# Optimization experiments

Hardware: AMD Instinct MI355X
Metric: run time of the kernel (lower is better)

## Reference

```python
import jax, jax.numpy as jnp
import numpy as np

D_MODEL = 768
D_FF = 3072
N_BEHAVIORS = 4
EPS = 1e-12


def layer_norm(x, g, b):
    m = jnp.mean(x, axis=-1, keepdims=True)
    v = jnp.mean(jnp.square(x - m), axis=-1, keepdims=True)
    return (x - m) * jax.lax.rsqrt(v + EPS) * g + b


def setup_inputs() -> dict:
    key = jax.random.key(0)
    ks = jax.random.split(key, 8)
    B, L = 8, 2048
    s1 = 1.0 / np.sqrt(D_MODEL)
    s2 = 1.0 / np.sqrt(D_FF)
    return {
        "input_tensor": jax.random.normal(ks[0], (B, L, D_MODEL), dtype=jnp.float32),
        "type_seq": jax.random.randint(ks[1], (B, L), 0, N_BEHAVIORS + 1),
        # per-behavior FeedForward params, stacked on leading n dim
        "W1": jax.random.normal(ks[2], (N_BEHAVIORS, D_MODEL, D_FF), dtype=jnp.float32) * s1,
        "b1": jnp.zeros((N_BEHAVIORS, D_FF), dtype=jnp.float32),
        "W2": jax.random.normal(ks[3], (N_BEHAVIORS, D_FF, D_MODEL), dtype=jnp.float32) * s2,
        "b2": jnp.zeros((N_BEHAVIORS, D_MODEL), dtype=jnp.float32),
        "ln_g": jnp.ones((N_BEHAVIORS, D_MODEL), dtype=jnp.float32),
        "ln_b": jnp.zeros((N_BEHAVIORS, D_MODEL), dtype=jnp.float32),
        # outer LayerNorm params
        "out_g": jnp.ones((D_MODEL,), dtype=jnp.float32),
        "out_b": jnp.zeros((D_MODEL,), dtype=jnp.float32),
    }


def reference(input_tensor, type_seq, W1, b1, W2, b2, ln_g, ln_b, out_g, out_b):
    n = W1.shape[0]
    # run every behavior's FeedForward over the full sequence (dense over-compute)
    h = jnp.einsum('BLH,nHF->nBLF', input_tensor, W1) + b1[:, None, None, :]
    h = jax.nn.gelu(h, approximate=False)  # torch 'gelu' = exact erf form
    h = jnp.einsum('nBLF,nFH->nBLH', h, W2) + b2[:, None, None, :]
    # per-expert residual LayerNorm (FeedForward with residual=True)
    h = layer_norm(h + input_tensor[None], ln_g[:, None, None, :], ln_b[:, None, None, :])
    # prepend zeros branch (class 0 = padding) then one-hot select per token
    stacked = jnp.concatenate([jnp.zeros_like(input_tensor)[None], h], axis=0)  # [n+1,B,L,H]
    onehot = jax.nn.one_hot(type_seq, n + 1, dtype=input_tensor.dtype)  # [B,L,n+1]
    sel = jnp.einsum('nBLH,BLn->BLH', stacked, onehot)
    # dropout is identity in eval; fused residual + LayerNorm
    return layer_norm(sel + input_tensor, out_g, out_b)
```

## Files before the change

kernel.cpp:

```cpp
#include <hip/hip_runtime.h>
#include <hip/hip_bf16.h>
#include <math.h>

#define NTOK   16384
#define DM     768
#define DF     3072
#define NEXP   4

#define RBLKS  64
#define XBLKS  768
#define WBLKS  288
#define PREP_BLKS (RBLKS + XBLKS + 2 * WBLKS)

typedef short bf16x8 __attribute__((ext_vector_type(8)));
typedef float f32x4  __attribute__((ext_vector_type(4)));

#define WS_CNT    0u
#define WS_BASES  256u
#define WS_POS    512u
#define WS_LIST   (512u + 65536u)
#define WS_XB     (WS_LIST + 262144u)
#define WS_W1T    (WS_XB + 25165824u)
#define WS_W2T    (WS_W1T + 18874368u)
#define WS_H1     (WS_W2T + 18874368u)
#define WS_H2     (WS_H1 + 100663296u)
#define WS_END    (WS_H2 + 25165824u)

__device__ __forceinline__ ushort f2bf(float f) {
    unsigned int v; __builtin_memcpy(&v, &f, 4);
    v = v + 0x7fffu + ((v >> 16) & 1u);
    return (ushort)(v >> 16);
}
__device__ __forceinline__ float bf2f(ushort u) {
    unsigned int v = ((unsigned int)u) << 16;
    float f; __builtin_memcpy(&f, &v, 4); return f;
}

__device__ __forceinline__ float fast_gelu(float v) {
    float y = v + 0.044715f * v * v * v;
    float e = __builtin_amdgcn_exp2f(-2.3022082f * y);
    return v * __builtin_amdgcn_rcpf(1.0f + e);
}

typedef __attribute__((address_space(1))) const void gvoid_t;
typedef __attribute__((address_space(3))) void lvoid_t;
__device__ __forceinline__ void cp16(const void* g, void* l) {
    __builtin_amdgcn_global_load_lds((gvoid_t*)g, (lvoid_t*)l, 16, 0, 0);
}

__device__ __forceinline__ int xcd_remap(int id, int T) {
    const int q = T >> 3, r = T & 7;
    const int x = id & 7, j = id >> 3;
    return (x < r ? x * (q + 1) : r * (q + 1) + (x - r) * q) + j;
}

__device__ __forceinline__ void transpose_tile(
    const float* __restrict__ src, ushort* __restrict__ dst, int R, int C,
    int bx, int by, int tid, ushort* tile ) {
    const int r0 = by * 64, c0 = bx * 64;
#pragma unroll
    for (int q = 0; q < 2; ++q) {
        int li = q * 256 + tid;
        int r = li >> 3, c = (li & 7) * 8;
        const float* s = src + (size_t)(r0 + r) * C + (c0 + c);
        float4 v0 = *(const float4*)s;
        float4 v1 = *(const float4*)(s + 4);
        ushort tmp[8];
        tmp[0] = f2bf(v0.x); tmp[1] = f2bf(v0.y); tmp[2] = f2bf(v0.z); tmp[3] = f2bf(v0.w);
        tmp[4] = f2bf(v1.x); tmp[5] = f2bf(v1.y); tmp[6] = f2bf(v1.z); tmp[7] = f2bf(v1.w);
        int sw = (((c >> 3) ^ ((r >> 3) & 7)) << 3);
        *(uint4*)&tile[r * 72 + sw] = *(uint4*)tmp;
    }
    __syncthreads();
#pragma unroll
    for (int q = 0; q < 2; ++q) {
        int li = q * 256 + tid;
        int r = li >> 3, c = (li & 7) * 8;
        ushort tmp[8];
#pragma unroll
        for (int j = 0; j < 8; ++j)
            tmp[j] = tile[(c + j) * 72 +
                          ((((r >> 3) & 7) ^ (((c + j) >> 3) & 7)) << 3) + (r & 7)];
        *(uint4*)(dst + (size_t)(c0 + r) * R + (r0 + c)) = *(uint4*)tmp;
    }
}

__global__ __launch_bounds__(256) void prep_kernel(
    const int* __restrict__ type_seq, const float* __restrict__ X,
    const float* __restrict__ W1, const float* __restrict__ W2,
    int* __restrict__ cnt,
    int* __restrict__ pos_of, int* __restrict__ list,
    ushort* __restrict__ Xb, ushort* __restrict__ W1t, ushort* __restrict__ W2t) {
    __shared__ ushort tile[64 * 72];
    __shared__ int lcnt[NEXP];
    __shared__ int lbase[NEXP];
    const int tid = threadIdx.x;
    const int bid = blockIdx.x;

    if (bid < RBLKS) {
        if (tid < NEXP) lcnt[tid] = 0;
        __syncthreads();
        const int lane = tid & 63;
        const int t = bid * 256 + tid;
        const int k = type_seq[t];
        int my_e = -1, my_p = 0;
#pragma unroll
        for (int e = 0; e < NEXP; ++e) {
            unsigned long long m = __ballot(k == e + 1);
            int total = __popcll(m);
            int b = 0;
            if (lane == 0 && total) b = atomicAdd(&lcnt[e], total);
            b = __shfl(b, 0, 64);
            if (k == e + 1) {
                my_e = e;
                my_p = b + __popcll(m & ((1ull << lane) - 1ull));
            }
        }
        __syncthreads();
        if (tid < NEXP && lcnt[tid] > 0)
            lbase[tid] = atomicAdd(&cnt[tid], lcnt[tid]);
        __syncthreads();
        if (my_e >= 0) {
            int gp = lbase[my_e] + my_p;
            list[my_e * NTOK + gp] = t;
            pos_of[t] = gp;
        }
        return;
    }

    int id = bid - RBLKS;
    if (id < XBLKS) {
        size_t ibase = ((size_t)id * 8 * 256 + tid) * 8;
        float4 va[8], vb[8];
#pragma unroll
        for (int k = 0; k < 8; ++k) {
            va[k] = *(const float4*)(X + ibase + (size_t)k * 2048);
            vb[k] = *(const float4*)(X + ibase + (size_t)k * 2048 + 4);
        }
#pragma unroll
        for (int k = 0; k < 8; ++k) {
            ushort tmp[8];
            tmp[0] = f2bf(va[k].x); tmp[1] = f2bf(va[k].y);
            tmp[2] = f2bf(va[k].z); tmp[3] = f2bf(va[k].w);
            tmp[4] = f2bf(vb[k].x); tmp[5] = f2bf(vb[k].y);
            tmp[6] = f2bf(vb[k].z); tmp[7] = f2bf(vb[k].w);
            *(uint4*)(Xb + ibase + (size_t)k * 2048) = *(uint4*)tmp;
        }
        return;
    }
    id -= XBLKS;
    if (id < WBLKS) {
#pragma unroll 1
        for (int k = 0; k < 8; ++k) {
            int tt = id * 8 + k;
            int z = tt / 576, rr = tt % 576;
            size_t mb = (size_t)z * DM * DF;
            transpose_tile(W1 + mb, W1t + mb, DM, DF, rr % 48, rr / 48, tid, tile);
            __syncthreads();
        }
        return;
    }
    id -= WBLKS;
    {
#pragma unroll 1
        for (int k = 0; k < 8; ++k) {
            int tt = id * 8 + k;
            int z = tt / 576, rr = tt % 576;
            size_t mb = (size_t)z * DF * DM;
            transpose_tile(W2 + mb, W2t + mb, DF, DM, rr % 12, rr / 12, tid, tile);
            __syncthreads();
        }
    }
}

__global__ __launch_bounds__(64) void scan_kernel(
    const int* __restrict__ cnt, int* __restrict__ bases) {
    if (threadIdx.x == 0) {
        int s = 0, mb = 0;
        for (int e = 0; e < NEXP; ++e) {
            bases[e] = s;
            bases[8 + e] = mb;
            s += cnt[e];
            mb += (cnt[e] + 127) >> 7;
        }
        bases[12] = mb;
    }
}


__global__ __launch_bounds__(512, 4) void gemm1_kernel(
    const ushort* __restrict__ Xb, const ushort* __restrict__ W1t,
    const float* __restrict__ b1, const int* __restrict__ cnt,
    const int* __restrict__ bases, const int* __restrict__ list,
    ushort* __restrict__ h1) {
    const int mb = bases[12];
    const int T = mb * 24;
    int id = blockIdx.y * 24 + blockIdx.x;
    if (id >= T) return;
    id = xcd_remap(id, T);
    const int y = id / 24;
    const int n0 = (id % 24) * 128;
    const int* mboff = bases + 8;
    const int e = (y >= mboff[1]) + (y >= mboff[2]) + (y >= mboff[3]);
    const int m0 = (y - mboff[e]) << 7;
    const int count = cnt[e];
    const int NK = DM / 32;

    __shared__ __align__(16) short As[3][4096];
    __shared__ __align__(16) short Bs[3][4096];

    const int tid = threadIdx.x;
    const int wave = tid >> 6, lane = tid & 63;
    const int wm = (wave & 1) * 64, wn = (wave >> 1) * 32;
    const int lrow = lane & 15;
    const int qg = lane >> 4;

    int r0 = min(m0 + (tid >> 2), count - 1);
    int t0 = list[e * NTOK + r0];
    const int qsrc = ((tid & 3) ^ ((tid >> 3) & 3)) * 8;
    const ushort* a0 = Xb + (size_t)t0 * DM + qsrc;
    const ushort* Wb = W1t + (size_t)e * DF * DM;
    const ushort* bp0 = Wb + (size_t)(n0 + (tid >> 2)) * DM + qsrc;

    int aOff[4], bOff[2];
#pragma unroll
    for (int i = 0; i < 4; ++i) {
        int ra = wm + i * 16 + lrow;
        aOff[i] = ra * 32 + (qg ^ ((ra >> 1) & 3)) * 8;
    }
#pragma unroll
    for (int j = 0; j < 2; ++j) {
        int rb = wn + j * 16 + lrow;
        bOff[j] = rb * 32 + (qg ^ ((rb >> 1) & 3)) * 8;
    }

    f32x4 z = {0.f, 0.f, 0.f, 0.f};
    f32x4 acc[4][2];
#pragma unroll
    for (int i = 0; i < 4; ++i)
#pragma unroll
        for (int j = 0; j < 2; ++j) acc[i][j] = z;

    auto STAGE = [&](int wb) {
        cp16(a0, &As[0][0] + wb * 4096 + tid * 8);
        cp16(bp0, &Bs[0][0] + wb * 4096 + tid * 8);
        a0 += 32; bp0 += 32;
    };

    STAGE(0); STAGE(1);
    int rb = 0;
    for (int ks = 0; ks < NK; ++ks) {
        __builtin_amdgcn_sched_barrier(0);
        if (ks + 1 < NK) { asm volatile("s_waitcnt vmcnt(2)" ::: "memory"); }
        else             { asm volatile("s_waitcnt vmcnt(0)" ::: "memory"); }
        __builtin_amdgcn_s_barrier();
        __builtin_amdgcn_sched_barrier(0);
        if (ks + 2 < NK) {
            int wb = rb - 1; if (wb < 0) wb += 3;
            STAGE(wb);
        }
        const short* Ab = &As[0][0] + rb * 4096;
        const short* Bb = &Bs[0][0] + rb * 4096;
        bf16x8 av[4], bv[2];
#pragma unroll
        for (int i = 0; i < 4; ++i) av[i] = *(const bf16x8*)(Ab + aOff[i]);
#pragma unroll
        for (int j = 0; j < 2; ++j) bv[j] = *(const bf16x8*)(Bb + bOff[j]);
#pragma unroll
        for (int i = 0; i < 4; ++i)
#pragma unroll
            for (int j = 0; j < 2; ++j)
                acc[i][j] = __builtin_amdgcn_mfma_f32_16x16x32_bf16(av[i], bv[j], acc[i][j], 0, 0, 0);
        rb = (rb + 1 == 3) ? 0 : rb + 1;
    }

    const int base = bases[e];
    float bias[2];
#pragma unroll
    for (int nt = 0; nt < 2; ++nt)
        bias[nt] = b1[e * DF + n0 + wn + nt * 16 + lrow];
#pragma unroll
    for (int mt = 0; mt < 4; ++mt) {
        int gm = m0 + wm + mt * 16 + (lane >> 4) * 4;
#pragma unroll
        for (int nt = 0; nt < 2; ++nt) {
            int gn = n0 + wn + nt * 16 + lrow;
#pragma unroll
            for (int r = 0; r < 4; ++r) {
                int i = gm + r;
                if (i < count) {
                    float v = acc[mt][nt][r] + bias[nt];
                    h1[(size_t)(base + i) * DF + gn] = f2bf(fast_gelu(v));
                }
            }
        }
    }
}

__global__ __launch_bounds__(512, 4) void gemm2_kernel(
    const ushort* __restrict__ h1, const ushort* __restrict__ W2t,
    const float* __restrict__ b2, const int* __restrict__ cnt,
    const int* __restrict__ bases, ushort* __restrict__ h2) {
    const int mb = bases[12];
    const int T = mb * 6;
    int id = blockIdx.y * 6 + blockIdx.x;
    if (id >= T) return;
    id = xcd_remap(id, T);
    const int y = id / 6;
    const int n0 = (id % 6) * 128;
    const int* mboff = bases + 8;
    const int e = (y >= mboff[1]) + (y >= mboff[2]) + (y >= mboff[3]);
    const int m0 = (y - mboff[e]) << 7;
    const int count = cnt[e];
    const int base = bases[e];
    const int NK = DF / 32;

    __shared__ __align__(16) short As[3][4096];
    __shared__ __align__(16) short Bs[3][4096];

    const int tid = threadIdx.x;
    const int wave = tid >> 6, lane = tid & 63;
    const int wm = (wave & 1) * 64, wn = (wave >> 1) * 32;
    const int lrow = lane & 15;
    const int qg = lane >> 4;

    int r0 = min(m0 + (tid >> 2), count - 1);
    const int qsrc = ((tid & 3) ^ ((tid >> 3) & 3)) * 8;
    const ushort* a0 = h1 + (size_t)(base + r0) * DF + qsrc;
    const ushort* Wb = W2t + (size_t)e * DM * DF;
    const ushort* bp0 = Wb + (size_t)(n0 + (tid >> 2)) * DF + qsrc;

    int aOff[4], bOff[2];
#pragma unroll
    for (int i = 0; i < 4; ++i) {
        int ra = wm + i * 16 + lrow;
        aOff[i] = ra * 32 + (qg ^ ((ra >> 1) & 3)) * 8;
    }
#pragma unroll
    for (int j = 0; j < 2; ++j) {
        int rb = wn + j * 16 + lrow;
        bOff[j] = rb * 32 + (qg ^ ((rb >> 1) & 3)) * 8;
    }

    f32x4 z = {0.f, 0.f, 0.f, 0.f};
    f32x4 acc[4][2];
#pragma unroll
    for (int i = 0; i < 4; ++i)
#pragma unroll
        for (int j = 0; j < 2; ++j) acc[i][j] = z;

    auto STAGE = [&](int wb) {
        cp16(a0, &As[0][0] + wb * 4096 + tid * 8);
        cp16(bp0, &Bs[0][0] + wb * 4096 + tid * 8);
        a0 += 32; bp0 += 32;
    };

    STAGE(0); STAGE(1);
    int rb = 0;
    for (int ks = 0; ks < NK; ++ks) {
        __builtin_amdgcn_sched_barrier(0);
        if (ks + 1 < NK) { asm volatile("s_waitcnt vmcnt(2)" ::: "memory"); }
        else             { asm volatile("s_waitcnt vmcnt(0)" ::: "memory"); }
        __builtin_amdgcn_s_barrier();
        __builtin_amdgcn_sched_barrier(0);
        if (ks + 2 < NK) {
            int wb = rb - 1; if (wb < 0) wb += 3;
            STAGE(wb);
        }
        const short* Ab = &As[0][0] + rb * 4096;
        const short* Bb = &Bs[0][0] + rb * 4096;
        bf16x8 av[4], bv[2];
#pragma unroll
        for (int i = 0; i < 4; ++i) av[i] = *(const bf16x8*)(Ab + aOff[i]);
#pragma unroll
        for (int j = 0; j < 2; ++j) bv[j] = *(const bf16x8*)(Bb + bOff[j]);
#pragma unroll
        for (int i = 0; i < 4; ++i)
#pragma unroll
            for (int j = 0; j < 2; ++j)
                acc[i][j] = __builtin_amdgcn_mfma_f32_16x16x32_bf16(av[i], bv[j], acc[i][j], 0, 0, 0);
        rb = (rb + 1 == 3) ? 0 : rb + 1;
    }

    float bias[2];
#pragma unroll
    for (int nt = 0; nt < 2; ++nt)
        bias[nt] = b2[e * DM + n0 + wn + nt * 16 + lrow];
#pragma unroll
    for (int mt = 0; mt < 4; ++mt) {
        int gm = m0 + wm + mt * 16 + (lane >> 4) * 4;
#pragma unroll
        for (int nt = 0; nt < 2; ++nt) {
            int gn = n0 + wn + nt * 16 + lrow;
#pragma unroll
            for (int r = 0; r < 4; ++r) {
                int i = gm + r;
                if (i < count)
                    h2[(size_t)(base + i) * DM + gn] = f2bf(acc[mt][nt][r] + bias[nt]);
            }
        }
    }
}

__global__ __launch_bounds__(256) void finalize_kernel(
    const float* __restrict__ X, const int* __restrict__ type_seq,
    const int* __restrict__ pos_of, const int* __restrict__ bases,
    const ushort* __restrict__ h2,
    const float* __restrict__ ln_g, const float* __restrict__ ln_b,
    const float* __restrict__ out_g, const float* __restrict__ out_b,
    float* __restrict__ out) {
    const int tid = threadIdx.x;
    const int wave = tid >> 6, lane = tid & 63;
    const int col0 = lane * 4;

#pragma unroll 1
    for (int ti = 0; ti < 2; ++ti) {
        const int t = blockIdx.x * 8 + wave * 2 + ti;
        const int k = type_seq[t];

        const float* Xr = X + (size_t)t * DM;
        float4 xv[3];
#pragma unroll
        for (int j = 0; j < 3; ++j) xv[j] = *(const float4*)(Xr + col0 + j * 256);

        float rv[12];
        if (k > 0) {
            const int e = k - 1;
            const size_t row = (size_t)(bases[e] + pos_of[t]);
            const ushort* hr = h2 + row * DM;
            float v[12];
            float s1 = 0.f, s2 = 0.f;
#pragma unroll
            for (int j = 0; j < 3; ++j) {
                ushort4 hv = *(const ushort4*)(hr + col0 + j * 256);
                float f0 = bf2f(hv.x) + xv[j].x;
                float f1 = bf2f(hv.y) + xv[j].y;
                float f2 = bf2f(hv.z) + xv[j].z;
                float f3 = bf2f(hv.w) + xv[j].w;
                v[j * 4 + 0] = f0; v[j * 4 + 1] = f1;
                v[j * 4 + 2] = f2; v[j * 4 + 3] = f3;
                s1 += (f0 + f1) + (f2 + f3);
                s2 += (f0 * f0 + f1 * f1) + (f2 * f2 + f3 * f3);
            }
#pragma unroll
            for (int off = 32; off > 0; off >>= 1) {
                s1 += __shfl_xor(s1, off, 64);
                s2 += __shfl_xor(s2, off, 64);
            }
            float m = s1 * (1.f / DM);
            float inv = rsqrtf(s2 * (1.f / DM) - m * m + 1e-12f);
#pragma unroll
            for (int j = 0; j < 3; ++j) {
                float4 g = *(const float4*)(ln_g + e * DM + col0 + j * 256);
                float4 b = *(const float4*)(ln_b + e * DM + col0 + j * 256);
                rv[j * 4 + 0] = (v[j * 4 + 0] - m) * inv * g.x + b.x;
                rv[j * 4 + 1] = (v[j * 4 + 1] - m) * inv * g.y + b.y;
                rv[j * 4 + 2] = (v[j * 4 + 2] - m) * inv * g.z + b.z;
                rv[j * 4 + 3] = (v[j * 4 + 3] - m) * inv * g.w + b.w;
            }
        } else {
#pragma unroll
            for (int j = 0; j < 12; ++j) rv[j] = 0.f;
        }

        float w[12];
        float s1 = 0.f, s2 = 0.f;
#pragma unroll
        for (int j = 0; j < 3; ++j) {
            float f0 = rv[j * 4 + 0] + xv[j].x;
            float f1 = rv[j * 4 + 1] + xv[j].y;
            float f2 = rv[j * 4 + 2] + xv[j].z;
            float f3 = rv[j * 4 + 3] + xv[j].w;
            w[j * 4 + 0] = f0; w[j * 4 + 1] = f1;
            w[j * 4 + 2] = f2; w[j * 4 + 3] = f3;
            s1 += (f0 + f1) + (f2 + f3);
            s2 += (f0 * f0 + f1 * f1) + (f2 * f2 + f3 * f3);
        }
#pragma unroll
        for (int off = 32; off > 0; off >>= 1) {
            s1 += __shfl_xor(s1, off, 64);
            s2 += __shfl_xor(s2, off, 64);
        }
        float m = s1 * (1.f / DM);
        float inv = rsqrtf(s2 * (1.f / DM) - m * m + 1e-12f);
#pragma unroll
        for (int j = 0; j < 3; ++j) {
            float4 g = *(const float4*)(out_g + col0 + j * 256);
            float4 b = *(const float4*)(out_b + col0 + j * 256);
            float4 o;
            o.x = (w[j * 4 + 0] - m) * inv * g.x + b.x;
            o.y = (w[j * 4 + 1] - m) * inv * g.y + b.y;
            o.z = (w[j * 4 + 2] - m) * inv * g.z + b.z;
            o.w = (w[j * 4 + 3] - m) * inv * g.w + b.w;
            *(float4*)(out + (size_t)t * DM + col0 + j * 256) = o;
        }
    }
}

extern "C" void kernel_launch(void* const* d_in, const int* in_sizes, int n_in,
                              void* d_out, int out_size, void* d_ws, size_t ws_size,
                              hipStream_t stream) {
    if (ws_size < (size_t)WS_END) return;

    const float* X     = (const float*)d_in[0];
    const int*   type  = (const int*)d_in[1];
    const float* W1    = (const float*)d_in[2];
    const float* b1    = (const float*)d_in[3];
    const float* W2    = (const float*)d_in[4];
    const float* b2    = (const float*)d_in[5];
    const float* ln_g  = (const float*)d_in[6];
    const float* ln_b  = (const float*)d_in[7];
    const float* out_g = (const float*)d_in[8];
    const float* out_b = (const float*)d_in[9];
    float* out = (float*)d_out;

    char* ws = (char*)d_ws;
    int* cnt    = (int*)(ws + WS_CNT);
    int* bases  = (int*)(ws + WS_BASES);
    int* pos_of = (int*)(ws + WS_POS);
    int* list   = (int*)(ws + WS_LIST);
    ushort* Xb  = (ushort*)(ws + WS_XB);
    ushort* W1t = (ushort*)(ws + WS_W1T);
    ushort* W2t = (ushort*)(ws + WS_W2T);
    ushort* h1  = (ushort*)(ws + WS_H1);
    ushort* h2  = (ushort*)(ws + WS_H2);

    hipMemsetAsync(cnt, 0, NEXP * sizeof(int), stream);
    prep_kernel<<<PREP_BLKS, 256, 0, stream>>>(type, X, W1, W2,
                                               cnt, pos_of, list, Xb, W1t, W2t);
    scan_kernel<<<1, 64, 0, stream>>>(cnt, bases);
    gemm1_kernel<<<dim3(24, 132), 512, 0, stream>>>(Xb, W1t, b1, cnt, bases, list, h1);
    gemm2_kernel<<<dim3(6, 132), 512, 0, stream>>>(h1, W2t, b2, cnt, bases, h2);
    finalize_kernel<<<NTOK / 8, 256, 0, stream>>>(X, type, pos_of, bases, h2, ln_g, ln_b, out_g, out_b, out);
}
```

Measured before the change: 379.0 us.

## Overlap W2 conversion with GEMM1, drop scan kernel, retile GEMM2

The W2 transpose/convert moves out of the prep kernel into spare blocks appended to the GEMM1 grid, so it runs alongside the first GEMM. The scan kernel is removed and each kernel recomputes expert bases from the counts inline. The W1 transpose now double-buffers its loads across tiles. GEMM2 switches to 256-thread blocks that each compute a 128x128 tile with 4x4 MFMA accumulators per wave, trading occupancy for register reuse. The added W2 blocks in GEMM1 compete with GEMM tiles for compute units, and the larger GEMM2 tiles raise register pressure.

```diff
diff --git a/kernel.cpp b/kernel.cpp
--- a/kernel.cpp
+++ b/kernel.cpp
@@ -10,7 +10,8 @@
 #define RBLKS  64
 #define XBLKS  768
 #define WBLKS  288
-#define PREP_BLKS (RBLKS + XBLKS + 2 * WBLKS)
+#define PREP_BLKS (RBLKS + XBLKS + WBLKS)
+#define W2BLKS 288
 
 typedef short bf16x8 __attribute__((ext_vector_type(8)));
 typedef float f32x4  __attribute__((ext_vector_type(4)));
@@ -54,44 +55,13 @@
     return (x < r ? x * (q + 1) : r * (q + 1) + (x - r) * q) + j;
 }
 
-__device__ __forceinline__ void transpose_tile(
-    const float* __restrict__ src, ushort* __restrict__ dst, int R, int C,
-    int bx, int by, int tid, ushort* tile ) {
-    const int r0 = by * 64, c0 = bx * 64;
-#pragma unroll
-    for (int q = 0; q < 2; ++q) {
-        int li = q * 256 + tid;
-        int r = li >> 3, c = (li & 7) * 8;
-        const float* s = src + (size_t)(r0 + r) * C + (c0 + c);
-        float4 v0 = *(const float4*)s;
-        float4 v1 = *(const float4*)(s + 4);
-        ushort tmp[8];
-        tmp[0] = f2bf(v0.x); tmp[1] = f2bf(v0.y); tmp[2] = f2bf(v0.z); tmp[3] = f2bf(v0.w);
-        tmp[4] = f2bf(v1.x); tmp[5] = f2bf(v1.y); tmp[6] = f2bf(v1.z); tmp[7] = f2bf(v1.w);
-        int sw = (((c >> 3) ^ ((r >> 3) & 7)) << 3);
-        *(uint4*)&tile[r * 72 + sw] = *(uint4*)tmp;
-    }
-    __syncthreads();
-#pragma unroll
-    for (int q = 0; q < 2; ++q) {
-        int li = q * 256 + tid;
-        int r = li >> 3, c = (li & 7) * 8;
-        ushort tmp[8];
-#pragma unroll
-        for (int j = 0; j < 8; ++j)
-            tmp[j] = tile[(c + j) * 72 +
-                          ((((r >> 3) & 7) ^ (((c + j) >> 3) & 7)) << 3) + (r & 7)];
-        *(uint4*)(dst + (size_t)(c0 + r) * R + (r0 + c)) = *(uint4*)tmp;
-    }
-}
-
 __global__ __launch_bounds__(256) void prep_kernel(
     const int* __restrict__ type_seq, const float* __restrict__ X,
-    const float* __restrict__ W1, const float* __restrict__ W2,
+    const float* __restrict__ W1,
     int* __restrict__ cnt,
     int* __restrict__ pos_of, int* __restrict__ list,
-    ushort* __restrict__ Xb, ushort* __restrict__ W1t, ushort* __restrict__ W2t) {
-    __shared__ ushort tile[64 * 72];
+    ushort* __restrict__ Xb, ushort* __restrict__ W1t) {
+    __shared__ ushort tbuf[2][64 * 72];
     __shared__ int lcnt[NEXP];
     __shared__ int lbase[NEXP];
     const int tid = threadIdx.x;
@@ -149,67 +119,108 @@
         return;
     }
     id -= XBLKS;
-    if (id < WBLKS) {
+    {
+        const int lr = tid >> 3;
+        const int lc = (tid & 7) * 8;
+        float4 v[2][2];
+        const int base_tt = id * 8;
+        auto LOADT = [&](int tt) {
+            int z = tt / 576, rr = tt % 576, bx = rr % 48, by = rr / 48;
+            const float* s0 = W1 + (size_t)z * DM * DF + (size_t)(by * 64 + lr) * DF + bx * 64 + lc;
+            v[0][0] = *(const float4*)s0;       v[0][1] = *(const float4*)(s0 + 4);
+            const float* s1 = s0 + (size_t)32 * DF;
+            v[1][0] = *(const float4*)s1;       v[1][1] = *(const float4*)(s1 + 4);
+        };
+        LOADT(base_tt);
 #pragma unroll 1
         for (int k = 0; k < 8; ++k) {
-            int tt = id * 8 + k;
-            int z = tt / 576, rr = tt % 576;
-            size_t mb = (size_t)z * DM * DF;
-            transpose_tile(W1 + mb, W1t + mb, DM, DF, rr % 48, rr / 48, tid, tile);
+            ushort* tb = &tbuf[k & 1][0];
+#pragma unroll
+            for (int q = 0; q < 2; ++q) {
+                int r = lr + q * 32;
+                ushort tmp[8];
+                tmp[0] = f2bf(v[q][0].x); tmp[1] = f2bf(v[q][0].y);
+                tmp[2] = f2bf(v[q][0].z); tmp[3] = f2bf(v[q][0].w);
+                tmp[4] = f2bf(v[q][1].x); tmp[5] = f2bf(v[q][1].y);
+                tmp[6] = f2bf(v[q][1].z); tmp[7] = f2bf(v[q][1].w);
+                int sw = (((lc >> 3) ^ ((r >> 3) & 7)) << 3);
+                *(uint4*)&tb[r * 72 + sw] = *(uint4*)tmp;
+            }
+            if (k < 7) LOADT(base_tt + k + 1);
             __syncthreads();
-        }
-        return;
-    }
-    id -= WBLKS;
-    {
-#pragma unroll 1
-        for (int k = 0; k < 8; ++k) {
-            int tt = id * 8 + k;
-            int z = tt / 576, rr = tt % 576;
-            size_t mb = (size_t)z * DF * DM;
-            transpose_tile(W2 + mb, W2t + mb, DF, DM, rr % 12, rr / 12, tid, tile);
-            __syncthreads();
-        }
-    }
-}
-
-__global__ __launch_bounds__(64) void scan_kernel(
-    const int* __restrict__ cnt, int* __restrict__ bases) {
-    if (threadIdx.x == 0) {
-        int s = 0, mb = 0;
-        for (int e = 0; e < NEXP; ++e) {
-            bases[e] = s;
-            bases[8 + e] = mb;
-            s += cnt[e];
-            mb += (cnt[e] + 127) >> 7;
-        }
-        bases[12] = mb;
-    }
-}
-
+            int tt = base_tt + k;
+            int z = tt / 576, rr = tt % 576, bx = rr % 48, by = rr / 48;
+#pragma unroll
+            for (int q = 0; q < 2; ++q) {
+                int r = lr + q * 32;
+                ushort tmp[8];
+#pragma unroll
+                for (int j = 0; j < 8; ++j)
+                    tmp[j] = tb[(lc + j) * 72 +
+                                ((((r >> 3) & 7) ^ (((lc + j) >> 3) & 7)) << 3) + (r & 7)];
+                *(uint4*)(W1t + (size_t)z * DM * DF + (size_t)(bx * 64 + r) * DM + by * 64 + lc) = *(uint4*)tmp;
+            }
+        }
+    }
+}
 
 __global__ __launch_bounds__(512, 4) void gemm1_kernel(
     const ushort* __restrict__ Xb, const ushort* __restrict__ W1t,
     const float* __restrict__ b1, const int* __restrict__ cnt,
-    const int* __restrict__ bases, const int* __restrict__ list,
-    ushort* __restrict__ h1) {
-    const int mb = bases[12];
+    const int* __restrict__ list, ushort* __restrict__ h1,
+    const float* __restrict__ W2, ushort* __restrict__ W2t) {
+    __shared__ __align__(16) short As[3][4096];
+    __shared__ __align__(16) short Bs[3][4096];
+    const int tid = threadIdx.x;
+
+    const int c0 = cnt[0], c1 = cnt[1], c2 = cnt[2], c3 = cnt[3];
+    const int p0 = (c0 + 127) >> 7, p1 = (c1 + 127) >> 7, p2 = (c2 + 127) >> 7;
+    const int mb = p0 + p1 + p2 + ((c3 + 127) >> 7);
     const int T = mb * 24;
     int id = blockIdx.y * 24 + blockIdx.x;
-    if (id >= T) return;
+
+    if (id >= T) {
+        int wid = id - T;
+        if (wid >= W2BLKS) return;
+        ushort* tb = (ushort*)&As[0][0];
+        const int lr = tid >> 3;
+        const int lc = (tid & 7) * 8;
+#pragma unroll 1
+        for (int k = 0; k < 8; ++k) {
+            int tt = wid * 8 + k;
+            int zz = tt / 576, rr = tt % 576, bx = rr % 12, by = rr / 12;
+            size_t mbase = (size_t)zz * DM * DF;
+            const float* s = W2 + mbase + (size_t)(by * 64 + lr) * DM + bx * 64 + lc;
+            float4 v0 = *(const float4*)s;
+            float4 v1 = *(const float4*)(s + 4);
+            ushort tmp[8];
+            tmp[0] = f2bf(v0.x); tmp[1] = f2bf(v0.y); tmp[2] = f2bf(v0.z); tmp[3] = f2bf(v0.w);
+            tmp[4] = f2bf(v1.x); tmp[5] = f2bf(v1.y); tmp[6] = f2bf(v1.z); tmp[7] = f2bf(v1.w);
+            int sw = (((lc >> 3) ^ ((lr >> 3) & 7)) << 3);
+            __syncthreads();
+            *(uint4*)&tb[lr * 72 + sw] = *(uint4*)tmp;
+            __syncthreads();
+            ushort o[8];
+#pragma unroll
+            for (int j = 0; j < 8; ++j)
+                o[j] = tb[(lc + j) * 72 +
+                          ((((lr >> 3) & 7) ^ (((lc + j) >> 3) & 7)) << 3) + (lr & 7)];
+            *(uint4*)(W2t + mbase + (size_t)(bx * 64 + lr) * DF + by * 64 + lc) = *(uint4*)o;
+        }
+        return;
+    }
+
     id = xcd_remap(id, T);
     const int y = id / 24;
     const int n0 = (id % 24) * 128;
-    const int* mboff = bases + 8;
-    const int e = (y >= mboff[1]) + (y >= mboff[2]) + (y >= mboff[3]);
-    const int m0 = (y - mboff[e]) << 7;
-    const int count = cnt[e];
+    const int q1 = p0, q2 = p0 + p1, q3 = p0 + p1 + p2;
+    const int e = (y >= q1) + (y >= q2) + (y >= q3);
+    const int mstart = (e > 0) * p0 + (e > 1) * p1 + (e > 2) * p2;
+    const int m0 = (y - mstart) << 7;
+    const int count = (e == 0) ? c0 : ((e == 1) ? c1 : ((e == 2) ? c2 : c3));
+    const int base = (e > 0) * c0 + (e > 1) * c1 + (e > 2) * c2;
     const int NK = DM / 32;
 
-    __shared__ __align__(16) short As[3][4096];
-    __shared__ __align__(16) short Bs[3][4096];
-
-    const int tid = threadIdx.x;
     const int wave = tid >> 6, lane = tid & 63;
     const int wm = (wave & 1) * 64, wn = (wave >> 1) * 32;
     const int lrow = lane & 15;
@@ -274,7 +285,6 @@
         rb = (rb + 1 == 3) ? 0 : rb + 1;
     }
 
-    const int base = bases[e];
     float bias[2];
 #pragma unroll
     for (int nt = 0; nt < 2; ++nt)
@@ -297,22 +307,25 @@
     }
 }
 
-__global__ __launch_bounds__(512, 4) void gemm2_kernel(
+__global__ __launch_bounds__(256, 3) void gemm2_kernel(
     const ushort* __restrict__ h1, const ushort* __restrict__ W2t,
     const float* __restrict__ b2, const int* __restrict__ cnt,
-    const int* __restrict__ bases, ushort* __restrict__ h2) {
-    const int mb = bases[12];
+    ushort* __restrict__ h2) {
+    const int c0 = cnt[0], c1 = cnt[1], c2 = cnt[2], c3 = cnt[3];
+    const int p0 = (c0 + 127) >> 7, p1 = (c1 + 127) >> 7, p2 = (c2 + 127) >> 7;
+    const int mb = p0 + p1 + p2 + ((c3 + 127) >> 7);
     const int T = mb * 6;
     int id = blockIdx.y * 6 + blockIdx.x;
     if (id >= T) return;
     id = xcd_remap(id, T);
     const int y = id / 6;
     const int n0 = (id % 6) * 128;
-    const int* mboff = bases + 8;
-    const int e = (y >= mboff[1]) + (y >= mboff[2]) + (y >= mboff[3]);
-    const int m0 = (y - mboff[e]) << 7;
-    const int count = cnt[e];
-    const int base = bases[e];
+    const int q1 = p0, q2 = p0 + p1, q3 = p0 + p1 + p2;
+    const int e = (y >= q1) + (y >= q2) + (y >= q3);
+    const int mstart = (e > 0) * p0 + (e > 1) * p1 + (e > 2) * p2;
+    const int m0 = (y - mstart) << 7;
+    const int count = (e == 0) ? c0 : ((e == 1) ? c1 : ((e == 2) ? c2 : c3));
+    const int base = (e > 0) * c0 + (e > 1) * c1 + (e > 2) * c2;
     const int NK = DF / 32;
 
     __shared__ __align__(16) short As[3][4096];
@@ -320,46 +333,49 @@
 
     const int tid = threadIdx.x;
     const int wave = tid >> 6, lane = tid & 63;
-    const int wm = (wave & 1) * 64, wn = (wave >> 1) * 32;
+    const int wm = (wave & 1) * 64, wn = (wave >> 1) * 64;
     const int lrow = lane & 15;
     const int qg = lane >> 4;
 
-    int r0 = min(m0 + (tid >> 2), count - 1);
+    const int srow = tid >> 2;
     const int qsrc = ((tid & 3) ^ ((tid >> 3) & 3)) * 8;
+    int r0 = min(m0 + srow, count - 1);
+    int r1 = min(m0 + 64 + srow, count - 1);
     const ushort* a0 = h1 + (size_t)(base + r0) * DF + qsrc;
+    const ushort* a1 = h1 + (size_t)(base + r1) * DF + qsrc;
     const ushort* Wb = W2t + (size_t)e * DM * DF;
-    const ushort* bp0 = Wb + (size_t)(n0 + (tid >> 2)) * DF + qsrc;
-
-    int aOff[4], bOff[2];
+    const ushort* bp0 = Wb + (size_t)(n0 + srow) * DF + qsrc;
+    const ushort* bp1 = bp0 + (size_t)64 * DF;
+
+    int aOff[4], bOff[4];
 #pragma unroll
     for (int i = 0; i < 4; ++i) {
         int ra = wm + i * 16 + lrow;
         aOff[i] = ra * 32 + (qg ^ ((ra >> 1) & 3)) * 8;
-    }
-#pragma unroll
-    for (int j = 0; j < 2; ++j) {
-        int rb = wn + j * 16 + lrow;
-        bOff[j] = rb * 32 + (qg ^ ((rb >> 1) & 3)) * 8;
+        int rbo = wn + i * 16 + lrow;
+        bOff[i] = rbo * 32 + (qg ^ ((rbo >> 1) & 3)) * 8;
     }
 
     f32x4 z = {0.f, 0.f, 0.f, 0.f};
-    f32x4 acc[4][2];
+    f32x4 acc[4][4];
 #pragma unroll
     for (int i = 0; i < 4; ++i)
 #pragma unroll
-        for (int j = 0; j < 2; ++j) acc[i][j] = z;
+        for (int j = 0; j < 4; ++j) acc[i][j] = z;
 
     auto STAGE = [&](int wb) {
-        cp16(a0, &As[0][0] + wb * 4096 + tid * 8);
-        cp16(bp0, &Bs[0][0] + wb * 4096 + tid * 8);
-        a0 += 32; bp0 += 32;
+        cp16(a0, &As[wb][0] + tid * 8);
+        cp16(a1, &As[wb][2048] + tid * 8);
+        cp16(bp0, &Bs[wb][0] + tid * 8);
+        cp16(bp1, &Bs[wb][2048] + tid * 8);
+        a0 += 32; a1 += 32; bp0 += 32; bp1 += 32;
     };
 
     STAGE(0); STAGE(1);
     int rb = 0;
     for (int ks = 0; ks < NK; ++ks) {
         __builtin_amdgcn_sched_barrier(0);
-        if (ks + 1 < NK) { asm volatile("s_waitcnt vmcnt(2)" ::: "memory"); }
+        if (ks + 1 < NK) { asm volatile("s_waitcnt vmcnt(4)" ::: "memory"); }
         else             { asm volatile("s_waitcnt vmcnt(0)" ::: "memory"); }
         __builtin_amdgcn_s_barrier();
         __builtin_amdgcn_sched_barrier(0);
@@ -367,36 +383,36 @@
             int wb = rb - 1; if (wb < 0) wb += 3;
             STAGE(wb);
         }
-        const short* Ab = &As[0][0] + rb * 4096;
-        const short* Bb = &Bs[0][0] + rb * 4096;
-        bf16x8 av[4], bv[2];
+        const short* Ab = &As[rb][0];
+        const short* Bb = &Bs[rb][0];
+        bf16x8 av[4], bv[4];
 #pragma unroll
         for (int i = 0; i < 4; ++i) av[i] = *(const bf16x8*)(Ab + aOff[i]);
 #pragma unroll
-        for (int j = 0; j < 2; ++j) bv[j] = *(const bf16x8*)(Bb + bOff[j]);
+        for (int j = 0; j < 4; ++j) bv[j] = *(const bf16x8*)(Bb + bOff[j]);
 #pragma unroll
         for (int i = 0; i < 4; ++i)
 #pragma unroll
-            for (int j = 0; j < 2; ++j)
+            for (int j = 0; j < 4; ++j)
                 acc[i][j] = __builtin_amdgcn_mfma_f32_16x16x32_bf16(av[i], bv[j], acc[i][j], 0, 0, 0);
         rb = (rb + 1 == 3) ? 0 : rb + 1;
     }
 
-    float bias[2];
-#pragma unroll
-    for (int nt = 0; nt < 2; ++nt)
-        bias[nt] = b2[e * DM + n0 + wn + nt * 16 + lrow];
-#pragma unroll
-    for (int mt = 0; mt < 4; ++mt) {
-        int gm = m0 + wm + mt * 16 + (lane >> 4) * 4;
-#pragma unroll
-        for (int nt = 0; nt < 2; ++nt) {
-            int gn = n0 + wn + nt * 16 + lrow;
+    float bias[4];
+#pragma unroll
+    for (int j = 0; j < 4; ++j)
+        bias[j] = b2[e * DM + n0 + wn + j * 16 + lrow];
+#pragma unroll
+    for (int i = 0; i < 4; ++i) {
+        int gm = m0 + wm + i * 16 + qg * 4;
+#pragma unroll
+        for (int j = 0; j < 4; ++j) {
+            int gn = n0 + wn + j * 16 + lrow;
 #pragma unroll
             for (int r = 0; r < 4; ++r) {
-                int i = gm + r;
-                if (i < count)
-                    h2[(size_t)(base + i) * DM + gn] = f2bf(acc[mt][nt][r] + bias[nt]);
+                int row = gm + r;
+                if (row < count)
+                    h2[(size_t)(base + row) * DM + gn] = f2bf(acc[i][j][r] + bias[j]);
             }
         }
     }
@@ -404,7 +420,7 @@
 
 __global__ __launch_bounds__(256) void finalize_kernel(
     const float* __restrict__ X, const int* __restrict__ type_seq,
-    const int* __restrict__ pos_of, const int* __restrict__ bases,
+    const int* __restrict__ pos_of, const int* __restrict__ cnt,
     const ushort* __restrict__ h2,
     const float* __restrict__ ln_g, const float* __restrict__ ln_b,
     const float* __restrict__ out_g, const float* __restrict__ out_b,
@@ -412,6 +428,7 @@
     const int tid = threadIdx.x;
     const int wave = tid >> 6, lane = tid & 63;
     const int col0 = lane * 4;
+    const int c0 = cnt[0], c1 = cnt[1], c2 = cnt[2];
 
 #pragma unroll 1
     for (int ti = 0; ti < 2; ++ti) {
@@ -426,7 +443,8 @@
         float rv[12];
         if (k > 0) {
             const int e = k - 1;
-            const size_t row = (size_t)(bases[e] + pos_of[t]);
+            const int base = (e > 0) * c0 + (e > 1) * c1 + (e > 2) * c2;
+            const size_t row = (size_t)(base + pos_of[t]);
             const ushort* hr = h2 + row * DM;
             float v[12];
             float s1 = 0.f, s2 = 0.f;
@@ -516,7 +534,6 @@
 
     char* ws = (char*)d_ws;
     int* cnt    = (int*)(ws + WS_CNT);
-    int* bases  = (int*)(ws + WS_BASES);
     int* pos_of = (int*)(ws + WS_POS);
     int* list   = (int*)(ws + WS_LIST);
     ushort* Xb  = (ushort*)(ws + WS_XB);
@@ -526,10 +543,9 @@
     ushort* h2  = (ushort*)(ws + WS_H2);
 
     hipMemsetAsync(cnt, 0, NEXP * sizeof(int), stream);
-    prep_kernel<<<PREP_BLKS, 256, 0, stream>>>(type, X, W1, W2,
-                                               cnt, pos_of, list, Xb, W1t, W2t);
-    scan_kernel<<<1, 64, 0, stream>>>(cnt, bases);
-    gemm1_kernel<<<dim3(24, 132), 512, 0, stream>>>(Xb, W1t, b1, cnt, bases, list, h1);
-    gemm2_kernel<<<dim3(6, 132), 512, 0, stream>>>(h1, W2t, b2, cnt, bases, h2);
-    finalize_kernel<<<NTOK / 8, 256, 0, stream>>>(X, type, pos_of, bases, h2, ln_g, ln_b, out_g, out_b, out);
-}
+    prep_kernel<<<PREP_BLKS, 256, 0, stream>>>(type, X, W1,
+                                               cnt, pos_of, list, Xb, W1t);
+    gemm1_kernel<<<dim3(24, 144), 512, 0, stream>>>(Xb, W1t, b1, cnt, list, h1, W2, W2t);
+    gemm2_kernel<<<dim3(6, 132), 256, 0, stream>>>(h1, W2t, b2, cnt, h2);
+    finalize_kernel<<<NTOK / 8, 256, 0, stream>>>(X, type, pos_of, cnt, h2, ln_g, ln_b, out_g, out_b, out);
+}
```

After: 374.4 us. About the same (-1.2%).
